# Performance work log

Measured on AMD Instinct MI355X. Metric: run time of the kernel, lower is better.

The kernel has to match this reference:

```python
import jax, jax.numpy as jnp
import numpy as np

B, CIN, COUT, K, H, W = 2, 128, 64, 64, 128, 128
BN_EPS = 1e-5


def setup_inputs() -> dict:
    key = jax.random.key(0)
    k1, k2, k3, k4 = jax.random.split(key, 4)
    x = jax.random.normal(k1, (B, CIN, H, W), dtype=jnp.float32)
    index = jax.random.randint(k2, (B, 1, H, W), 0, K)  # superpixel labels
    # kaiming_uniform(a=sqrt(5)) ~ uniform with bound sqrt(6/((1+5)*fan_in)) = 1/sqrt(fan_in)
    Wft = jax.random.uniform(k3, (CIN, COUT), dtype=jnp.float32,
                             minval=-1.0, maxval=1.0) / np.sqrt(CIN).astype(np.float32)
    Wm = jax.random.uniform(k4, (COUT, COUT), dtype=jnp.float32,
                            minval=-1.0, maxval=1.0) / np.sqrt(COUT).astype(np.float32)
    gamma = jnp.ones((COUT,), jnp.float32)
    beta = jnp.zeros((COUT,), jnp.float32)
    return {"x": x, "index": index, "Wft": Wft, "Wm": Wm, "gamma": gamma, "beta": beta}


def _gnn_forward(x, index, Wft, Wm, gamma, beta):
    # FeatureTransform: [B,Cin,H,W] -> [B,Cout,H,W]
    xt = jnp.einsum('bchw,co->bohw', x, Wft)

    idx = index[:, 0]                                   # [B,H,W]
    oh = jax.nn.one_hot(idx, K, dtype=xt.dtype)         # [B,H,W,K]

    # RegionalMeans (segment-mean over superpixels; equivalent to the
    # repeated-tensor multiply+sum in the torch code, without the 5D blowup)
    block_sum = oh.sum(axis=(1, 2))                     # [B,K]
    sums = jnp.einsum('bhwk,bohw->bko', oh, xt)         # [B,K,Cout]
    denom = block_sum + (block_sum == 0).astype(xt.dtype)
    means = sums / denom[..., None]                     # [B,K,Cout]

    # Adj: pairwise Mahalanobis distance with learned cov = Wm @ Wm.T
    cov = Wm @ Wm.T
    inv_cov = jnp.linalg.inv(cov)
    diff = means[:, :, None, :] - means[:, None, :, :]  # [B,K,K,Cout]
    q = jnp.einsum('bijc,cd,bijd->bij', diff, inv_cov, diff)
    dist = jnp.sqrt(jnp.maximum(q, 1e-12))              # clamp: diagonal q==0
    adj = jnp.exp(-dist)                                # [B,K,K]

    # GCN propagate: adjacency-weighted aggregation of region means
    adj_means = jnp.einsum('bij,bjo->bio', adj, means)  # [B,K,Cout]

    # sum_k one_hot_k * (x_rep + adj_means_k) == xt + gather(adj_means, idx)
    gathered = jnp.take_along_axis(adj_means, idx.reshape(B, -1, 1), axis=1)
    gathered = gathered.reshape(B, H, W, COUT).transpose(0, 3, 1, 2)
    features = jax.nn.relu(xt + gathered)               # [B,Cout,H,W]

    # BatchNorm2d (training-mode batch statistics, biased variance)
    mean = features.mean(axis=(0, 2, 3), keepdims=True)
    var = features.var(axis=(0, 2, 3), keepdims=True)
    out = (features - mean) / jnp.sqrt(var + BN_EPS)
    out = out * gamma[None, :, None, None] + beta[None, :, None, None]
    return out


def reference(x, index, Wft, Wm, gamma, beta):
    return _gnn_forward(x, index, Wft, Wm, gamma, beta)
```

## Files before the change

### kernel.cpp

```cpp
#include <hip/hip_runtime.h>
#include <hip/hip_bf16.h>

#define CIN   128
#define COUT  64
#define HW    16384

typedef __hip_bfloat16 bf16;

#define OFF_XT    0u
#define OFF_PS    1048576u
#define OFF_PC    2097152u
#define OFF_MEANS 2129920u
#define OFF_DIAG  2138112u
#define OFF_INV   2138240u
#define OFF_ADJM  2142336u
#define OFF_BNP   2150528u

__device__ __forceinline__ unsigned short f2bfu(float f) {
  union { bf16 h; unsigned short u; } cv; cv.h = __float2bfloat16(f); return cv.u;
}
__device__ __forceinline__ float bf2f(unsigned short u) {
  union { unsigned int i; float f; } cv; cv.i = ((unsigned int)u) << 16; return cv.f;
}

__global__ __launch_bounds__(256, 2) void k1_xt_bins_inv(
    const float* __restrict__ x, const int* __restrict__ index,
    const float* __restrict__ Wft, const float* __restrict__ Wm,
    float* __restrict__ ws)
{
  __shared__ __align__(16) float smem[16384];
  const int blk = blockIdx.x, tid = threadIdx.x;
  if (blk != 0) {
    float* xl = smem;
    float* wl = smem + 8192;
    const int eb = blk - 1;
    const int b = eb >> 8, ps = eb & 255;
    const float* xg = x + (size_t)b * CIN * HW + ps * 64;
#pragma unroll
    for (int j = 0; j < 8; ++j) {
      const int fj = j * 256 + tid;
      const int c = fj >> 4, q4 = (fj & 15) * 4;
      *(float4*)&xl[c * 64 + q4] = *(const float4*)(xg + (size_t)c * HW + q4);
      *(float4*)&wl[c * 64 + q4] = *(const float4*)(Wft + c * 64 + q4);
    }
    __syncthreads();
    const int px_grp = tid & 15, o_grp = tid >> 4;
    const int px = ps * 64 + px_grp * 4, o0 = o_grp * 4;
    float acc[16];
#pragma unroll
    for (int j = 0; j < 16; ++j) acc[j] = 0.f;
#pragma unroll 8
    for (int c = 0; c < 128; ++c) {
      const float4 xv = *(const float4*)&xl[c * 64 + px_grp * 4];
      const float4 wv = *(const float4*)&wl[c * 64 + o0];
      acc[ 0]=fmaf(xv.x,wv.x,acc[ 0]); acc[ 1]=fmaf(xv.y,wv.x,acc[ 1]);
      acc[ 2]=fmaf(xv.z,wv.x,acc[ 2]); acc[ 3]=fmaf(xv.w,wv.x,acc[ 3]);
      acc[ 4]=fmaf(xv.x,wv.y,acc[ 4]); acc[ 5]=fmaf(xv.y,wv.y,acc[ 5]);
      acc[ 6]=fmaf(xv.z,wv.y,acc[ 6]); acc[ 7]=fmaf(xv.w,wv.y,acc[ 7]);
      acc[ 8]=fmaf(xv.x,wv.z,acc[ 8]); acc[ 9]=fmaf(xv.y,wv.z,acc[ 9]);
      acc[10]=fmaf(xv.z,wv.z,acc[10]); acc[11]=fmaf(xv.w,wv.z,acc[11]);
      acc[12]=fmaf(xv.x,wv.w,acc[12]); acc[13]=fmaf(xv.y,wv.w,acc[13]);
      acc[14]=fmaf(xv.z,wv.w,acc[14]); acc[15]=fmaf(xv.w,wv.w,acc[15]);
    }
    unsigned short* xtu = (unsigned short*)(ws + OFF_XT);
#pragma unroll
    for (int oj = 0; oj < 4; ++oj) {
      ushort4 u;
      u.x = f2bfu(acc[oj*4+0]); u.y = f2bfu(acc[oj*4+1]);
      u.z = f2bfu(acc[oj*4+2]); u.w = f2bfu(acc[oj*4+3]);
      *(ushort4*)(xtu + (size_t)(b * 64 + o0 + oj) * HW + px) = u;
    }
    const int4 kv = *(const int4*)(index + b * HW + px);
    const int kk[4] = {kv.x, kv.y, kv.z, kv.w};
    __syncthreads();
    float* bins = smem;
    float* cnt  = smem + 64 * 68;
    for (int i = tid; i < 64 * 68 + 64; i += 256) smem[i] = 0.f;
    __syncthreads();
#pragma unroll
    for (int pj = 0; pj < 4; ++pj) {
      const int kb = kk[pj] * 68 + o0;
      atomicAdd(&bins[kb    ], acc[ 0 + pj]);
      atomicAdd(&bins[kb + 1], acc[ 4 + pj]);
      atomicAdd(&bins[kb + 2], acc[ 8 + pj]);
      atomicAdd(&bins[kb + 3], acc[12 + pj]);
    }
    if (o_grp == 0) {
#pragma unroll
      for (int pj = 0; pj < 4; ++pj) atomicAdd(&cnt[kk[pj]], 1.f);
    }
    __syncthreads();
    unsigned short* pb = (unsigned short*)(ws + OFF_PS) + (size_t)eb * 4096;
    {
      const int k = tid >> 2, ob = (tid & 3) * 16;
#pragma unroll
      for (int q = 0; q < 4; ++q) {
        const float4 v = *(const float4*)&bins[k * 68 + ob + q * 4];
        ushort4 u;
        u.x = f2bfu(v.x); u.y = f2bfu(v.y); u.z = f2bfu(v.z); u.w = f2bfu(v.w);
        *(ushort4*)(pb + k * 64 + ob + q * 4) = u;
      }
    }
    if (tid < 64) ws[OFF_PC + (size_t)(b * 64 + tid) * 256 + ps] = cnt[tid];
  } else {
    float* wm = smem;
    float* pr = smem + 8192;
    float* pc = smem + 8320;
    for (int e = tid; e < 4096; e += 256) wm[(e >> 6) * 68 + (e & 63)] = Wm[e];
    __syncthreads();
    const int ig = tid >> 4, jg = tid & 15;
    const int i0 = ig << 2, j0 = jg << 2;
    float c4[16];
#pragma unroll
    for (int q = 0; q < 16; ++q) c4[q] = 0.f;
    for (int cq = 0; cq < 64; cq += 4) {
      float4 a[4], bb[4];
#pragma unroll
      for (int ii = 0; ii < 4; ++ii) a[ii]  = *(const float4*)&wm[(i0+ii)*68 + cq];
#pragma unroll
      for (int jj = 0; jj < 4; ++jj) bb[jj] = *(const float4*)&wm[(j0+jj)*68 + cq];
#pragma unroll
      for (int ii = 0; ii < 4; ++ii)
#pragma unroll
        for (int jj = 0; jj < 4; ++jj)
          c4[ii*4+jj] = fmaf(a[ii].x, bb[jj].x, fmaf(a[ii].y, bb[jj].y,
                        fmaf(a[ii].z, bb[jj].z, fmaf(a[ii].w, bb[jj].w, c4[ii*4+jj]))));
    }
    __syncthreads();
    __builtin_amdgcn_s_setprio(3);
    int buf = 0;
#pragma unroll 1
    for (int k = 0; k < 64; ++k) {
      const int kg = k >> 2, kr = k & 3;
      if (ig == kg) {
        pr[buf * 64 + j0 + 0] = c4[kr * 4 + 0];
        pr[buf * 64 + j0 + 1] = c4[kr * 4 + 1];
        pr[buf * 64 + j0 + 2] = c4[kr * 4 + 2];
        pr[buf * 64 + j0 + 3] = c4[kr * 4 + 3];
      }
      if (jg == kg) {
        pc[buf * 64 + i0 + 0] = c4[0 * 4 + kr];
        pc[buf * 64 + i0 + 1] = c4[1 * 4 + kr];
        pc[buf * 64 + i0 + 2] = c4[2 * 4 + kr];
        pc[buf * 64 + i0 + 3] = c4[3 * 4 + kr];
      }
      __syncthreads();
      const float rp = __builtin_amdgcn_rcpf(pr[buf * 64 + k]);
      float s[4], ai[4];
#pragma unroll
      for (int jj = 0; jj < 4; ++jj) s[jj] = pr[buf * 64 + j0 + jj];
#pragma unroll
      for (int ii = 0; ii < 4; ++ii)
        ai[ii] = (i0 + ii == k) ? (rp - 1.0f) : (-pc[buf * 64 + i0 + ii] * rp);
#pragma unroll
      for (int ii = 0; ii < 4; ++ii)
#pragma unroll
        for (int jj = 0; jj < 4; ++jj)
          c4[ii*4+jj] = fmaf(ai[ii], s[jj], c4[ii*4+jj]);
      if (jg == kg) {
#pragma unroll
        for (int ii = 0; ii < 4; ++ii)
          c4[ii*4+kr] = (i0 + ii == k) ? rp : ai[ii];
      }
      buf ^= 1;
    }
    __builtin_amdgcn_s_setprio(0);
#pragma unroll
    for (int ii = 0; ii < 4; ++ii)
#pragma unroll
      for (int jj = 0; jj < 4; ++jj)
        ws[OFF_INV + (size_t)(i0 + ii) * 64 + j0 + jj] = c4[ii*4+jj];
  }
}

__global__ __launch_bounds__(1024) void k15_means_diag(float* __restrict__ ws)
{
  __shared__ float red[1024];
  __shared__ float lds_c[4];
  __shared__ float lds_m[64];
  const int blk = blockIdx.x, t = threadIdx.x;
  const int b = blk >> 6, k = blk & 63;
  const int o = t & 63, chunk = t >> 6;
  const unsigned short* psu = (const unsigned short*)(ws + OFF_PS);
  float s = 0.f;
#pragma unroll
  for (int i = 0; i < 16; ++i) {
    const int slab = chunk * 16 + i;
    s += bf2f(psu[(size_t)(b * 256 + slab) * 4096 + k * 64 + o]);
  }
  red[chunk * 64 + o] = s;
  float cv = 0.f;
  if (t < 256) cv = ws[OFF_PC + (size_t)(b * 64 + k) * 256 + t];
#pragma unroll
  for (int m = 32; m; m >>= 1) cv += __shfl_xor(cv, m, 64);
  if (t < 256 && (t & 63) == 0) lds_c[t >> 6] = cv;
  __syncthreads();
  if (t < 64) {
    float m_raw = 0.f;
#pragma unroll
    for (int ch = 0; ch < 16; ++ch) m_raw += red[ch * 64 + o];
    const float cnt = lds_c[0] + lds_c[1] + lds_c[2] + lds_c[3];
    const float denom = cnt + ((cnt == 0.f) ? 1.f : 0.f);
    const float m = m_raw / denom;
    ws[OFF_MEANS + (size_t)(b * 64 + k) * 64 + o] = m;
    lds_m[o] = m;
    float inner = 0.f;
#pragma unroll 8
    for (int d = 0; d < 64; ++d) inner = fmaf(ws[OFF_INV + d * 64 + o], lds_m[d], inner);
    float p = m * inner;
#pragma unroll
    for (int mm = 32; mm; mm >>= 1) p += __shfl_xor(p, mm, 64);
    if (o == 0) ws[OFF_DIAG + b * 64 + k] = p;
  }
}

__global__ __launch_bounds__(256) void k2_adj(float* __restrict__ ws)
{
  __shared__ __align__(16) float means_s[64 * 68];
  __shared__ __align__(16) float inv_s[64 * 68];
  __shared__ __align__(16) float T_s[8 * 68];
  __shared__ __align__(16) float adj_s[8 * 68];
  __shared__ float diag_s[64];
  const int b = blockIdx.x >> 3;
  const int i0 = (blockIdx.x & 7) << 3;
  const int t = threadIdx.x;
  const float* mg = ws + OFF_MEANS + b * 4096;
  for (int e = t; e < 4096; e += 256) means_s[(e >> 6) * 68 + (e & 63)] = mg[e];
  const float* ig = ws + OFF_INV;
  for (int e = t; e < 4096; e += 256) inv_s[(e >> 6) * 68 + (e & 63)] = ig[e];
  if (t < 64) diag_s[t] = ws[OFF_DIAG + b * 64 + t];
  __syncthreads();
  if (t < 128) {
    const int i = t >> 4, d0 = (t & 15) << 2;
    float4 acc = {0.f, 0.f, 0.f, 0.f};
    for (int c = 0; c < 64; ++c) {
      const float mv = means_s[(i0 + i) * 68 + c];
      const float4 iv = *(const float4*)&inv_s[c * 68 + d0];
      acc.x = fmaf(mv, iv.x, acc.x); acc.y = fmaf(mv, iv.y, acc.y);
      acc.z = fmaf(mv, iv.z, acc.z); acc.w = fmaf(mv, iv.w, acc.w);
    }
    *(float4*)&T_s[i * 68 + d0] = acc;
  }
  __syncthreads();
  {
    const int i = t >> 5, jb = t & 31;
#pragma unroll
    for (int jj = 0; jj < 2; ++jj) {
      const int j = jb + (jj << 5);
      float4 p4 = {0.f, 0.f, 0.f, 0.f};
      for (int dq = 0; dq < 64; dq += 4) {
        const float4 tv = *(const float4*)&T_s[i * 68 + dq];
        const float4 mv = *(const float4*)&means_s[j * 68 + dq];
        p4.x = fmaf(tv.x, mv.x, p4.x); p4.y = fmaf(tv.y, mv.y, p4.y);
        p4.z = fmaf(tv.z, mv.z, p4.z); p4.w = fmaf(tv.w, mv.w, p4.w);
      }
      const float p = (p4.x + p4.y) + (p4.z + p4.w);
      const float q = diag_s[i0 + i] + diag_s[j] - 2.f * p;
      adj_s[i * 68 + j] = __expf(-sqrtf(fmaxf(q, 1e-12f)));
    }
  }
  __syncthreads();
  if (t < 128) {
    const int i = t >> 4, oq = (t & 15) << 2;
    float4 am = {0.f, 0.f, 0.f, 0.f};
    for (int j = 0; j < 64; ++j) {
      const float av = adj_s[i * 68 + j];
      const float4 mv = *(const float4*)&means_s[j * 68 + oq];
      am.x = fmaf(av, mv.x, am.x); am.y = fmaf(av, mv.y, am.y);
      am.z = fmaf(av, mv.z, am.z); am.w = fmaf(av, mv.w, am.w);
    }
    *(float4*)(ws + OFF_ADJM + (size_t)(b * 64 + i0 + i) * 64 + oq) = am;
  }
}

__global__ __launch_bounds__(256) void k3_bnstats(const int* __restrict__ index,
                                                  float* __restrict__ ws)
{
  __shared__ float am_s[128];
  __shared__ float red[4];
  const int blk = blockIdx.x, t = threadIdx.x;
  const int b = blk >> 8, oc = (blk >> 3) & 31, tile = blk & 7;
  const int o0 = oc * 2;
  if (t < 128) am_s[t] = ws[OFF_ADJM + (size_t)(b * 64 + (t >> 1)) * 64 + o0 + (t & 1)];
  if (t < 4) red[t] = 0.f;
  __syncthreads();
  const int lane = t & 63, w = t >> 6;
  const unsigned short* xtu = (const unsigned short*)(ws + OFF_XT);
  float s0 = 0.f, s1 = 0.f, q0 = 0.f, q1 = 0.f;
#pragma unroll
  for (int q = 0; q < 2; ++q) {
    const int px = tile * 2048 + (w * 2 + q) * 256 + lane * 4;
    const int4 kv = *(const int4*)(index + b * HW + px);
    const ushort4 u0 = *(const ushort4*)(xtu + (size_t)(b * 64 + o0    ) * HW + px);
    const ushort4 u1 = *(const ushort4*)(xtu + (size_t)(b * 64 + o0 + 1) * HW + px);
    const int kk[4] = {kv.x, kv.y, kv.z, kv.w};
    const float x0[4] = {bf2f(u0.x), bf2f(u0.y), bf2f(u0.z), bf2f(u0.w)};
    const float x1[4] = {bf2f(u1.x), bf2f(u1.y), bf2f(u1.z), bf2f(u1.w)};
#pragma unroll
    for (int j = 0; j < 4; ++j) {
      const float2 am = *(const float2*)&am_s[kk[j] * 2];
      const float f0 = fmaxf(x0[j] + am.x, 0.f);
      const float f1 = fmaxf(x1[j] + am.y, 0.f);
      s0 += f0; q0 = fmaf(f0, f0, q0);
      s1 += f1; q1 = fmaf(f1, f1, q1);
    }
  }
#pragma unroll
  for (int m = 1; m < 64; m <<= 1) {
    s0 += __shfl_xor(s0, m, 64); s1 += __shfl_xor(s1, m, 64);
    q0 += __shfl_xor(q0, m, 64); q1 += __shfl_xor(q1, m, 64);
  }
  if (lane == 0) {
    atomicAdd(&red[0], s0); atomicAdd(&red[1], s1);
    atomicAdd(&red[2], q0); atomicAdd(&red[3], q1);
  }
  __syncthreads();
  if (t == 0) {
    float4 v; v.x = red[0]; v.y = red[1]; v.z = red[2]; v.w = red[3];
    *(float4*)(ws + OFF_BNP + (size_t)(oc * 16 + b * 8 + tile) * 4) = v;
  }
}

__global__ __launch_bounds__(256) void k4_out(const int* __restrict__ index,
    const float* __restrict__ gamma, const float* __restrict__ beta,
    const float* __restrict__ ws, float* __restrict__ out)
{
  __shared__ float am_s[128];
  __shared__ float4 tmp[16];
  __shared__ float sc_s[2], sh_s[2];
  const int blk = blockIdx.x, t = threadIdx.x;
  const int b = blk >> 8, oc = (blk >> 3) & 31, tile = blk & 7;
  const int o0 = oc * 2;
  if (t < 128) am_s[t] = ws[OFF_ADJM + (size_t)(b * 64 + (t >> 1)) * 64 + o0 + (t & 1)];
  if (t < 16) tmp[t] = *(const float4*)(ws + OFF_BNP + (size_t)(oc * 16 + t) * 4);
  if (t < 2) {
    float s = 0.f, qq = 0.f;
#pragma unroll
    for (int i = 0; i < 16; ++i) {
      const float4 v = tmp[i];
      s  += (t == 0) ? v.x : v.y;
      qq += (t == 0) ? v.z : v.w;
    }
    const float mean = s * (1.f / 32768.f);
    const float var  = qq * (1.f / 32768.f) - mean * mean;
    const float sc = gamma[o0 + t] * rsqrtf(var + 1e-5f);
    sc_s[t] = sc;
    sh_s[t] = fmaf(-mean, sc, beta[o0 + t]);
  }
  __syncthreads();
  const int lane = t & 63, w = t >> 6;
  const unsigned short* xtu = (const unsigned short*)(ws + OFF_XT);
  const float c0 = sc_s[0], c1 = sc_s[1], h0 = sh_s[0], h1 = sh_s[1];
#pragma unroll
  for (int q = 0; q < 2; ++q) {
    const int px = tile * 2048 + (w * 2 + q) * 256 + lane * 4;
    const int4 kv = *(const int4*)(index + b * HW + px);
    const ushort4 u0 = *(const ushort4*)(xtu + (size_t)(b * 64 + o0    ) * HW + px);
    const ushort4 u1 = *(const ushort4*)(xtu + (size_t)(b * 64 + o0 + 1) * HW + px);
    const int kk[4] = {kv.x, kv.y, kv.z, kv.w};
    const float x0[4] = {bf2f(u0.x), bf2f(u0.y), bf2f(u0.z), bf2f(u0.w)};
    const float x1[4] = {bf2f(u1.x), bf2f(u1.y), bf2f(u1.z), bf2f(u1.w)};
    float4 o4a, o4b;
    float* oa = (float*)&o4a; float* ob = (float*)&o4b;
#pragma unroll
    for (int j = 0; j < 4; ++j) {
      const float2 am = *(const float2*)&am_s[kk[j] * 2];
      oa[j] = fmaf(fmaxf(x0[j] + am.x, 0.f), c0, h0);
      ob[j] = fmaf(fmaxf(x1[j] + am.y, 0.f), c1, h1);
    }
    *(float4*)(out + (size_t)(b * 64 + o0    ) * HW + px) = o4a;
    *(float4*)(out + (size_t)(b * 64 + o0 + 1) * HW + px) = o4b;
  }
}

extern "C" void kernel_launch(void* const* d_in, const int* in_sizes, int n_in,
                              void* d_out, int out_size, void* d_ws, size_t ws_size,
                              hipStream_t stream) {
  const float* x     = (const float*)d_in[0];
  const int*   index = (const int*)d_in[1];
  const float* Wft   = (const float*)d_in[2];
  const float* Wm    = (const float*)d_in[3];
  const float* gamma = (const float*)d_in[4];
  const float* beta  = (const float*)d_in[5];
  float* ws  = (float*)d_ws;
  float* out = (float*)d_out;

  k1_xt_bins_inv<<<513, 256, 0, stream>>>(x, index, Wft, Wm, ws);
  k15_means_diag<<<128, 1024, 0, stream>>>(ws);
  k2_adj<<<16, 256, 0, stream>>>(ws);
  k3_bnstats<<<512, 256, 0, stream>>>(index, ws);
  k4_out<<<512, 256, 0, stream>>>(index, gamma, beta, ws, out);
}
```

Before: 129.8 us.

## Block the in-place Gauss-Jordan matrix inverse into 4x4 pivot panels

Replaces the 64-step scalar-pivot Gauss-Jordan inversion of the 64x64 covariance with a 16-step blocked version. Each step inverts a 4x4 diagonal block redundantly per thread and applies rank-4 Schur-complement updates to the register tiles. This cuts the number of block-wide barriers and LDS round-trips by four and uses float4 LDS accesses. The cost is more arithmetic per step and more registers for the dd/cc/rr/T arrays. Accuracy may drift slightly because pivots are taken within blocks.

New measurement: 120.1 us. 7.5% less time.

```diff
diff --git a/kernel.cpp b/kernel.cpp
--- a/kernel.cpp
+++ b/kernel.cpp
@@ -104,8 +104,8 @@
     if (tid < 64) ws[OFF_PC + (size_t)(b * 64 + tid) * 256 + ps] = cnt[tid];
   } else {
     float* wm = smem;
-    float* pr = smem + 8192;
-    float* pc = smem + 8320;
+    float* Rb = smem + 8192;
+    float* Cb = smem + 8704;
     for (int e = tid; e < 4096; e += 256) wm[(e >> 6) * 68 + (e & 63)] = Wm[e];
     __syncthreads();
     const int ig = tid >> 4, jg = tid & 15;
@@ -130,37 +130,87 @@
     __builtin_amdgcn_s_setprio(3);
     int buf = 0;
 #pragma unroll 1
-    for (int k = 0; k < 64; ++k) {
-      const int kg = k >> 2, kr = k & 3;
-      if (ig == kg) {
-        pr[buf * 64 + j0 + 0] = c4[kr * 4 + 0];
-        pr[buf * 64 + j0 + 1] = c4[kr * 4 + 1];
-        pr[buf * 64 + j0 + 2] = c4[kr * 4 + 2];
-        pr[buf * 64 + j0 + 3] = c4[kr * 4 + 3];
-      }
-      if (jg == kg) {
-        pc[buf * 64 + i0 + 0] = c4[0 * 4 + kr];
-        pc[buf * 64 + i0 + 1] = c4[1 * 4 + kr];
-        pc[buf * 64 + i0 + 2] = c4[2 * 4 + kr];
-        pc[buf * 64 + i0 + 3] = c4[3 * 4 + kr];
+    for (int p = 0; p < 16; ++p) {
+      const int P = p << 2;
+      float* Rp = Rb + buf * 256;
+      float* Cp = Cb + buf * 256;
+      if (ig == p) {
+#pragma unroll
+        for (int r = 0; r < 4; ++r) {
+          float4 t; t.x = c4[r*4+0]; t.y = c4[r*4+1]; t.z = c4[r*4+2]; t.w = c4[r*4+3];
+          *(float4*)&Rp[r * 64 + j0] = t;
+        }
+      }
+      if (jg == p) {
+#pragma unroll
+        for (int ii = 0; ii < 4; ++ii) {
+          float4 t; t.x = c4[ii*4+0]; t.y = c4[ii*4+1]; t.z = c4[ii*4+2]; t.w = c4[ii*4+3];
+          *(float4*)&Cp[(i0 + ii) * 4] = t;
+        }
       }
       __syncthreads();
-      const float rp = __builtin_amdgcn_rcpf(pr[buf * 64 + k]);
-      float s[4], ai[4];
-#pragma unroll
-      for (int jj = 0; jj < 4; ++jj) s[jj] = pr[buf * 64 + j0 + jj];
+      float dd[16], cc[16], rr[16];
+#pragma unroll
+      for (int r = 0; r < 4; ++r) *(float4*)&dd[r * 4] = *(const float4*)&Rp[r * 64 + P];
+#pragma unroll
+      for (int ii = 0; ii < 4; ++ii) *(float4*)&cc[ii * 4] = *(const float4*)&Cp[(i0 + ii) * 4];
+#pragma unroll
+      for (int r = 0; r < 4; ++r) *(float4*)&rr[r * 4] = *(const float4*)&Rp[r * 64 + j0];
+#pragma unroll
+      for (int k = 0; k < 4; ++k) {
+        const float rp = __builtin_amdgcn_rcpf(dd[k * 4 + k]);
+        float ai[4], s[4];
+#pragma unroll
+        for (int j = 0; j < 4; ++j) s[j] = dd[k * 4 + j];
+#pragma unroll
+        for (int i = 0; i < 4; ++i) ai[i] = (i == k) ? (rp - 1.0f) : (-dd[i * 4 + k] * rp);
+#pragma unroll
+        for (int i = 0; i < 4; ++i)
+#pragma unroll
+          for (int j = 0; j < 4; ++j) dd[i * 4 + j] = fmaf(ai[i], s[j], dd[i * 4 + j]);
+#pragma unroll
+        for (int i = 0; i < 4; ++i) dd[i * 4 + k] = (i == k) ? rp : ai[i];
+      }
+      float T[16];
 #pragma unroll
       for (int ii = 0; ii < 4; ++ii)
-        ai[ii] = (i0 + ii == k) ? (rp - 1.0f) : (-pc[buf * 64 + i0 + ii] * rp);
-#pragma unroll
-      for (int ii = 0; ii < 4; ++ii)
-#pragma unroll
-        for (int jj = 0; jj < 4; ++jj)
-          c4[ii*4+jj] = fmaf(ai[ii], s[jj], c4[ii*4+jj]);
-      if (jg == kg) {
+#pragma unroll
+        for (int c = 0; c < 4; ++c) {
+          float t = cc[ii*4+0] * dd[0*4+c];
+          t = fmaf(cc[ii*4+1], dd[1*4+c], t);
+          t = fmaf(cc[ii*4+2], dd[2*4+c], t);
+          t = fmaf(cc[ii*4+3], dd[3*4+c], t);
+          T[ii*4+c] = t;
+        }
+      if (ig == p && jg == p) {
+#pragma unroll
+        for (int q = 0; q < 16; ++q) c4[q] = dd[q];
+      } else if (ig == p) {
+#pragma unroll
+        for (int r = 0; r < 4; ++r)
+#pragma unroll
+          for (int jj = 0; jj < 4; ++jj) {
+            float t = dd[r*4+0] * rr[0*4+jj];
+            t = fmaf(dd[r*4+1], rr[1*4+jj], t);
+            t = fmaf(dd[r*4+2], rr[2*4+jj], t);
+            t = fmaf(dd[r*4+3], rr[3*4+jj], t);
+            c4[r*4+jj] = t;
+          }
+      } else if (jg == p) {
+#pragma unroll
+        for (int q = 0; q < 16; ++q) c4[q] = -T[q];
+      } else {
 #pragma unroll
         for (int ii = 0; ii < 4; ++ii)
-          c4[ii*4+kr] = (i0 + ii == k) ? rp : ai[ii];
+#pragma unroll
+          for (int jj = 0; jj < 4; ++jj) {
+            float t = c4[ii*4+jj];
+            t = fmaf(-T[ii*4+0], rr[0*4+jj], t);
+            t = fmaf(-T[ii*4+1], rr[1*4+jj], t);
+            t = fmaf(-T[ii*4+2], rr[2*4+jj], t);
+            t = fmaf(-T[ii*4+3], rr[3*4+jj], t);
+            c4[ii*4+jj] = t;
+          }
       }
       buf ^= 1;
     }
```
